# Kernel tuning notes

Hardware: AMD Instinct MI355X
Metric: run time of the kernel (lower is better)

The kernel has to match this reference:

```python
import jax, jax.numpy as jnp
import numpy as np

N_NODES = 100000
N_EDGES = 3200000
N_GRAPHS = 128
HIDDEN = 128
DEPTH = 3


def setup_inputs() -> dict:
    key = jax.random.key(0)
    ks = jax.random.split(key, 12)
    x = jax.random.normal(ks[0], (N_NODES, 1), dtype=jnp.float32)
    edge_index = jax.random.randint(ks[1], (2, N_EDGES), 0, N_NODES, dtype=jnp.int64)
    batch = jnp.sort(jax.random.randint(ks[2], (N_NODES,), 0, N_GRAPHS, dtype=jnp.int64))
    s = 1.0 / np.sqrt(HIDDEN)
    return {
        "x": x,
        "edge_index": edge_index,
        "batch": batch,
        "W_emb": jax.random.normal(ks[3], (1, HIDDEN), dtype=jnp.float32),
        "b_emb": jax.random.normal(ks[4], (HIDDEN,), dtype=jnp.float32) * 0.01,
        "W_gnn": jax.random.normal(ks[5], (DEPTH, HIDDEN, HIDDEN), dtype=jnp.float32) * s,
        "b_gnn": jax.random.normal(ks[6], (DEPTH, HIDDEN), dtype=jnp.float32) * 0.01,
        "W_c1": jax.random.normal(ks[7], (HIDDEN, HIDDEN // 2), dtype=jnp.float32) * s,
        "b_c1": jax.random.normal(ks[8], (HIDDEN // 2,), dtype=jnp.float32) * 0.01,
        "W_c2": jax.random.normal(ks[9], (HIDDEN // 2, 1), dtype=jnp.float32) * s,
        "b_c2": jax.random.normal(ks[10], (1,), dtype=jnp.float32) * 0.01,
    }


def reference(x, edge_index, batch, W_emb, b_emb, W_gnn, b_gnn, W_c1, b_c1, W_c2, b_c2):
    # --- GCN normalization (self-loops + symmetric deg^-1/2) ---
    loop = jnp.arange(N_NODES, dtype=edge_index.dtype)
    row = jnp.concatenate([edge_index[0], loop])  # source nodes
    col = jnp.concatenate([edge_index[1], loop])  # target nodes
    deg = jax.ops.segment_sum(jnp.ones_like(col, dtype=jnp.float32), col, num_segments=N_NODES)
    dinv = jnp.where(deg > 0, jax.lax.rsqrt(jnp.maximum(deg, 1.0)), 0.0)
    norm = dinv[row] * dinv[col]  # [E+N]

    # --- node embedding ---
    h = x @ W_emb + b_emb  # [N, H]

    # --- GCN layers: linear -> gather -> normalize -> scatter-add -> bias -> relu ---
    for l in range(DEPTH):
        h_lin = h @ W_gnn[l]                       # [N, H]
        msgs = h_lin[row] * norm[:, None]          # [E+N, H]
        agg = jax.ops.segment_sum(msgs, col, num_segments=N_NODES)
        h = jax.nn.relu(agg + b_gnn[l])

    # --- global mean pool per graph ---
    counts = jax.ops.segment_sum(jnp.ones((N_NODES,), jnp.float32), batch, num_segments=N_GRAPHS)
    sums = jax.ops.segment_sum(h, batch, num_segments=N_GRAPHS)
    g = sums / jnp.maximum(counts, 1.0)[:, None]   # [G, H]

    # --- classifier (dropout is identity in eval) ---
    z = jax.nn.relu(g @ W_c1 + b_c1)
    out = jax.nn.sigmoid(z @ W_c2 + b_c2)          # [G, 1]
    return out.squeeze(-1)                          # [G]
```

## Files before the change

### kernel.cpp

```cpp
#include <hip/hip_runtime.h>
#include <math.h>

#define HID 128
#define CAP 96
#define TILE 2048
#define WCAP 6144

typedef unsigned int uint;
typedef unsigned short ushort;
typedef float f32x2 __attribute__((ext_vector_type(2)));
typedef float f32x4 __attribute__((ext_vector_type(4)));
typedef short bf16x8 __attribute__((ext_vector_type(8)));

__device__ inline ushort f2bf(float f) {
    uint u = __float_as_uint(f);
    return (ushort)((u + 0x7fffu + ((u >> 16) & 1u)) >> 16);
}
__device__ inline uint packbf(float a, float b) {
    return (uint)f2bf(a) | ((uint)f2bf(b) << 16);
}

__device__ inline f32x2 fp8lo(uint q) { return __builtin_amdgcn_cvt_pk_f32_fp8(q, false); }
__device__ inline f32x2 fp8hi(uint q) { return __builtin_amdgcn_cvt_pk_f32_fp8(q, true); }
__device__ inline uint pack4fp8(float a, float b, float c, float d) {
    int t = __builtin_amdgcn_cvt_pk_fp8_f32(a, b, 0, false);
    return (uint)__builtin_amdgcn_cvt_pk_fp8_f32(c, d, t, true);
}
__device__ inline long long as_i64(uint2 u) {
    union { uint2 a; long long b; } c;
    c.a = u;
    return c.b;
}


__global__ void __launch_bounds__(256) k_part(const int* __restrict__ row,
                                              const int* __restrict__ col,
                                              int* __restrict__ bukCur,
                                              uint* __restrict__ recs, int E, int nTiles,
                                              const float* __restrict__ W_emb,
                                              const float* __restrict__ b_emb,
                                              const float* __restrict__ W_gnn,
                                              float* __restrict__ u, float* __restrict__ v,
                                              uint2* __restrict__ wfrag) {
    __shared__ int hist[800];
    __shared__ int hist2[800];
    __shared__ uint base[800];
    int t = threadIdx.x;
    if ((int)blockIdx.x >= nTiles) {
        int b = blockIdx.x - nTiles;
        if (b < 16) {
            int gid = b * 256 + t;
            int l = gid >> 11;
            int rem = gid & 2047;
            int kb = rem >> 9;
            int nt = (rem >> 6) & 7;
            int lane = rem & 63;
            int k0 = kb * 32 + (lane >> 4) * 8;
            int n = nt * 16 + (lane & 15);
            const float* Wp = W_gnn + (size_t)(l + 1) * HID * HID;
            uint2 o;
            o.x = pack4fp8(Wp[(k0 + 0) * HID + n], Wp[(k0 + 1) * HID + n],
                           Wp[(k0 + 2) * HID + n], Wp[(k0 + 3) * HID + n]);
            o.y = pack4fp8(Wp[(k0 + 4) * HID + n], Wp[(k0 + 5) * HID + n],
                           Wp[(k0 + 6) * HID + n], Wp[(k0 + 7) * HID + n]);
            wfrag[gid] = o;
        } else if (t < HID) {
            float su = 0.f, sv = 0.f;
            for (int k = 0; k < HID; ++k) {
                float w = W_gnn[k * HID + t];
                su = fmaf(W_emb[k], w, su);
                sv = fmaf(b_emb[k], w, sv);
            }
            u[t] = su;
            v[t] = sv;
        }
        return;
    }
    for (int i = t; i < 800; i += 256) { hist[i] = 0; hist2[i] = 0; }
    __syncthreads();
    int i0 = blockIdx.x * TILE;
    int i1 = min(E, i0 + TILE);
    for (int i = i0 + t; i < i1; i += 256) {
        atomicAdd(&hist[col[i] >> 7], 1);
    }
    __syncthreads();
    for (int i = t; i < 800; i += 256)
        if (hist[i] > 0) base[i] = (uint)atomicAdd(&bukCur[i], hist[i]);
    __syncthreads();
    for (int i = i0 + t; i < i1; i += 256) {
        int c = col[i];
        int w = c >> 7;
        uint p = (uint)atomicAdd(&hist2[w], 1);
        uint idx = base[w] + p;
        if (idx < WCAP)
            recs[(size_t)w * WCAP + idx] = (uint)row[i] | ((uint)(c & 127) << 17);
    }
}


__global__ void __launch_bounds__(256) k_fbin(const uint* __restrict__ recs,
                                              const int* __restrict__ bukCur,
                                              const float* __restrict__ x,
                                              int* __restrict__ cnt,
                                              int* __restrict__ ebin,
                                              float* __restrict__ dinv,
                                              float2* __restrict__ pk0, int N) {
    __shared__ int lcnt[128];
    int w = blockIdx.x;
    int t = threadIdx.x;
    if (t < 128) lcnt[t] = 0;
    __syncthreads();
    int n = min(bukCur[w], WCAP);
    const uint* rp = recs + (size_t)w * WCAP;
    int cbase = w << 7;
    for (int j = t; j < n; j += 256) {
        uint u = rp[j];
        int r = (int)(u & 0x1FFFFu);
        int cl = (int)((u >> 17) & 127u);
        int p = atomicAdd(&lcnt[cl], 1);
        if (p < CAP) ebin[(size_t)(cbase + cl) * CAP + p] = r << 5;
    }
    __syncthreads();
    if (t < 128) {
        int c = cbase + t;
        if (c < N) {
            cnt[c] = lcnt[t];
            float d = rsqrtf((float)lcnt[t] + 1.0f);
            dinv[c] = d;
            pk0[c] = make_float2(d, d * x[c]);
        }
    }
}


__global__ void __launch_bounds__(256) k_sagg(const int* __restrict__ cnt,
                                              const int* __restrict__ ebin,
                                              const float* __restrict__ x,
                                              const float* __restrict__ dinv,
                                              const float2* __restrict__ pk0,
                                              const float* __restrict__ u,
                                              const float* __restrict__ v,
                                              const float* __restrict__ b0,
                                              uint* __restrict__ g8, int N) {
    __shared__ float sS0[16], sS1[16], sDc[16];
    int t = threadIdx.x;
    int qw = t >> 4;
    int ll = t & 15;
    int c0 = blockIdx.x * 16;
    int c = c0 + qw;
    float A = 0.f, B = 0.f;
    float dc = 0.f;
    if (c < N) {
        dc = dinv[c];
        int n = min(cnt[c], CAP);
        const int* bp = ebin + (size_t)c * CAP;
        int k = ll;
        for (; k + 16 < n; k += 32) {
            int o0 = bp[k], o1 = bp[k + 16];
            float2 p0 = pk0[o0 >> 5], p1 = pk0[o1 >> 5];
            A += p0.x + p1.x;
            B += p0.y + p1.y;
        }
        if (k < n) {
            float2 p = pk0[bp[k] >> 5];
            A += p.x;
            B += p.y;
        }
    }
#pragma unroll
    for (int m = 1; m <= 8; m <<= 1) {
        A += __shfl_xor(A, m);
        B += __shfl_xor(B, m);
    }
    if (ll == 0 && c < N) {
        float d2 = dc * dc;
        sS0[qw] = fmaf(dc, A, d2);
        sS1[qw] = fmaf(dc, B, d2 * x[c]);
        sDc[qw] = dc;
    }
    __syncthreads();
    int nloc = min(16, N - c0);
    int total = nloc * 32;
    for (int gid = t; gid < total; gid += 256) {
        int lc = gid >> 5;
        int j = (gid & 31) * 4;
        float t1 = sS1[lc], t0 = sS0[lc], dcc = sDc[lc];
        float v0 = fmaxf(fmaf(t1, u[j + 0], fmaf(t0, v[j + 0], b0[j + 0])), 0.f);
        float v1 = fmaxf(fmaf(t1, u[j + 1], fmaf(t0, v[j + 1], b0[j + 1])), 0.f);
        float v2 = fmaxf(fmaf(t1, u[j + 2], fmaf(t0, v[j + 2], b0[j + 2])), 0.f);
        float v3 = fmaxf(fmaf(t1, u[j + 3], fmaf(t0, v[j + 3], b0[j + 3])), 0.f);
        g8[(size_t)(c0 + lc) * 32 + (gid & 31)] = pack4fp8(dcc * v0, dcc * v1, dcc * v2, dcc * v3);
    }
}


__global__ void __launch_bounds__(256) k_agg(const int* __restrict__ cnt,
                                             const int* __restrict__ ebin,
                                             const float* __restrict__ dinv,
                                             const uint* __restrict__ g8,
                                             uint* __restrict__ a, int N) {
    int wave = (blockIdx.x * 256 + threadIdx.x) >> 6;
    if (wave >= N) return;
    int lane = threadIdx.x & 63;
    int c = wave;
    int ql = lane & 15;
    int qg = lane >> 4;
    const uint* __restrict__ gq = g8 + ql * 2;

    f32x2 a0 = {0.f, 0.f}, a1 = {0.f, 0.f}, a2 = {0.f, 0.f}, a3 = {0.f, 0.f};

    int n = min(cnt[c], CAP);
    int total = n + 1;
    const int* __restrict__ bp = ebin + (size_t)c * CAP - 1;

    for (int base = 0; base < total; base += 64) {
        int cw = min(total - base, 64);
        int gi = base + lane;
        int ro = 0;
        if (lane < cw) ro = (gi == 0) ? (c << 5) : bp[gi];
        int j = 0;
        for (; j + 16 <= cw; j += 16) {
            int o0 = __shfl(ro, j + qg);
            int o1 = __shfl(ro, j + 4 + qg);
            int o2 = __shfl(ro, j + 8 + qg);
            int o3 = __shfl(ro, j + 12 + qg);
            uint2 q0 = *(const uint2*)(gq + o0);
            uint2 q1 = *(const uint2*)(gq + o1);
            uint2 q2 = *(const uint2*)(gq + o2);
            uint2 q3 = *(const uint2*)(gq + o3);
            a0 += fp8lo(q0.x); a1 += fp8hi(q0.x); a2 += fp8lo(q0.y); a3 += fp8hi(q0.y);
            a0 += fp8lo(q1.x); a1 += fp8hi(q1.x); a2 += fp8lo(q1.y); a3 += fp8hi(q1.y);
            a0 += fp8lo(q2.x); a1 += fp8hi(q2.x); a2 += fp8lo(q2.y); a3 += fp8hi(q2.y);
            a0 += fp8lo(q3.x); a1 += fp8hi(q3.x); a2 += fp8lo(q3.y); a3 += fp8hi(q3.y);
        }
        for (; j + 4 <= cw; j += 4) {
            int o0 = __shfl(ro, j + qg);
            uint2 q0 = *(const uint2*)(gq + o0);
            a0 += fp8lo(q0.x); a1 += fp8hi(q0.x); a2 += fp8lo(q0.y); a3 += fp8hi(q0.y);
        }
        if (j < cw) {
            int e = j + qg;
            int o0 = __shfl(ro, min(e, cw - 1));
            uint2 q0 = *(const uint2*)(gq + o0);
            if (e >= cw) { q0.x = 0u; q0.y = 0u; }
            a0 += fp8lo(q0.x); a1 += fp8hi(q0.x); a2 += fp8lo(q0.y); a3 += fp8hi(q0.y);
        }
    }

    float r0 = a0.x, r1 = a0.y, r2 = a1.x, r3 = a1.y;
    float r4 = a2.x, r5 = a2.y, r6 = a3.x, r7 = a3.y;
#pragma unroll
    for (int m = 16; m <= 32; m <<= 1) {
        r0 += __shfl_xor(r0, m); r1 += __shfl_xor(r1, m);
        r2 += __shfl_xor(r2, m); r3 += __shfl_xor(r3, m);
        r4 += __shfl_xor(r4, m); r5 += __shfl_xor(r5, m);
        r6 += __shfl_xor(r6, m); r7 += __shfl_xor(r7, m);
    }
    if (qg == 0) {
        float dc = dinv[c];
        uint2 o;
        o.x = pack4fp8(dc * r0, dc * r1, dc * r2, dc * r3);
        o.y = pack4fp8(dc * r4, dc * r5, dc * r6, dc * r7);
        ((uint2*)(a + (size_t)c * 32))[ql] = o;
    }
}


#define RCH 32
__global__ void __launch_bounds__(256, 2) k_gemm(const uint* __restrict__ A,
                                                 const uint2* __restrict__ wfrag,
                                                 const float* __restrict__ bias,
                                                 const float* __restrict__ rowscale,
                                                 uint* __restrict__ H8, int N) {
    __shared__ uint2 sAf[4][2][64];
    __shared__ float sEp[4][16][68];
    int t = threadIdx.x;
    int w = t >> 6;
    int lane = t & 63;
    int rowgrp = w >> 1;
    int colh = w & 1;

    uint2 Bf[4][4];
#pragma unroll
    for (int kb = 0; kb < 4; ++kb)
#pragma unroll
        for (int i = 0; i < 4; ++i)
            Bf[kb][i] = wfrag[(kb * 8 + colh * 4 + i) * 64 + lane];

    float4 bb = ((const float4*)bias)[colh * 16 + (lane & 15)];

    int nchunk = (N + RCH - 1) / RCH;
    for (int ch = blockIdx.x; ch < nchunk; ch += gridDim.x) {
        int r0 = ch * RCH;
        __syncthreads();
        {
            int i = t;
#pragma unroll
            for (int s = 0; s < 2; ++s, i += 256) {
                int kb = i >> 7;
                int rg = (i >> 6) & 1;
                int ln = i & 63;
                int gr = r0 + rg * 16 + (ln & 15);
                gr = min(gr, N - 1);
                sAf[kb][rg][ln] = ((const uint2*)(A + (size_t)gr * 32))[kb * 4 + (ln >> 4)];
            }
        }
        __syncthreads();

        f32x4 acc[4] = {{0.f, 0.f, 0.f, 0.f}, {0.f, 0.f, 0.f, 0.f},
                        {0.f, 0.f, 0.f, 0.f}, {0.f, 0.f, 0.f, 0.f}};
#pragma unroll
        for (int kb = 0; kb < 4; ++kb) {
            long long af = as_i64(sAf[kb][rowgrp][lane]);
#pragma unroll
            for (int i = 0; i < 4; ++i)
                acc[i] = __builtin_amdgcn_mfma_f32_16x16x32_fp8_fp8(af, as_i64(Bf[kb][i]),
                                                                    acc[i], 0, 0, 0);
        }

#pragma unroll
        for (int i = 0; i < 4; ++i) {
#pragma unroll
            for (int reg = 0; reg < 4; ++reg)
                sEp[w][(lane >> 4) * 4 + reg][i * 16 + (lane & 15)] = acc[i][reg];
        }
#pragma unroll
        for (int e = 0; e < 4; ++e) {
            int rr = (lane >> 4) + 4 * e;
            int cu = lane & 15;
            const float* sp = &sEp[w][rr][cu * 4];
            int rowg = r0 + rowgrp * 16 + rr;
            if (rowg < N) {
                float sc = rowscale ? rowscale[rowg] : 1.0f;
                float o0 = sc * fmaxf(sp[0] + bb.x, 0.f);
                float o1 = sc * fmaxf(sp[1] + bb.y, 0.f);
                float o2 = sc * fmaxf(sp[2] + bb.z, 0.f);
                float o3 = sc * fmaxf(sp[3] + bb.w, 0.f);
                H8[(size_t)rowg * 32 + colh * 16 + cu] = pack4fp8(o0, o1, o2, o3);
            }
        }
    }
}



__global__ void k_pool(const uint* __restrict__ h8, const int* __restrict__ batch,
                       float* __restrict__ gpp, float* __restrict__ gcnt, int N) {
    __shared__ float sp[128];
    int gi = blockIdx.x >> 2, part = blockIdx.x & 3;
    int G = gridDim.x >> 2;
    int t = threadIdx.x;
    int ui = t & 31;
    int sub = t >> 5;
    sp[t] = 0.f;
    __syncthreads();
    int lo = 0, hi = N;
    while (lo < hi) { int m = (lo + hi) >> 1; if (batch[m] < gi) lo = m + 1; else hi = m; }
    int start = lo;
    lo = start; hi = N;
    while (lo < hi) { int m = (lo + hi) >> 1; if (batch[m] <= gi) lo = m + 1; else hi = m; }
    int end = lo;
    if (part == 0 && t == 0) gcnt[gi] = (float)(end - start);
    int len = end - start;
    int q = (len + 15) >> 4;
    int seg = part * 4 + sub;
    int rs = start + seg * q;
    int re = min(end, rs + q);
    float s0 = 0.f, s1 = 0.f, s2 = 0.f, s3 = 0.f;
    for (int i = rs; i < re; ++i) {
        uint qq = h8[(size_t)i * 32 + ui];
        f32x2 lo2 = fp8lo(qq), hi2 = fp8hi(qq);
        s0 += lo2.x; s1 += lo2.y; s2 += hi2.x; s3 += hi2.y;
    }
    if (re > rs) {
        atomicAdd(&sp[ui * 4 + 0], s0);
        atomicAdd(&sp[ui * 4 + 1], s1);
        atomicAdd(&sp[ui * 4 + 2], s2);
        atomicAdd(&sp[ui * 4 + 3], s3);
    }
    __syncthreads();
    gpp[((size_t)part * G + gi) * 128 + t] = sp[t];
}

__global__ void k_cls(const float* __restrict__ gpp, const float* __restrict__ gcnt,
                      const float* __restrict__ Wc1, const float* __restrict__ bc1,
                      const float* __restrict__ Wc2, const float* __restrict__ bc2,
                      float* __restrict__ out, int G) {
    __shared__ float sg[128];
    int g = blockIdx.x;
    int j = threadIdx.x;
    float inv = 1.0f / fmaxf(gcnt[g], 1.0f);
    for (int k = j; k < 128; k += 64) {
        float s = gpp[((size_t)0 * G + g) * 128 + k] + gpp[((size_t)1 * G + g) * 128 + k] +
                  gpp[((size_t)2 * G + g) * 128 + k] + gpp[((size_t)3 * G + g) * 128 + k];
        sg[k] = s * inv;
    }
    __syncthreads();
    float z = bc1[j];
    for (int k = 0; k < HID; ++k) z = fmaf(sg[k], Wc1[k * 64 + j], z);
    z = fmaxf(z, 0.f);
    float p = z * Wc2[j];
    for (int off = 32; off; off >>= 1) p += __shfl_down(p, off);
    if (j == 0) out[g] = 1.0f / (1.0f + expf(-(p + bc2[0])));
}


extern "C" void kernel_launch(void* const* d_in, const int* in_sizes, int n_in,
                              void* d_out, int out_size, void* d_ws, size_t ws_size,
                              hipStream_t stream) {
    const float* x     = (const float*)d_in[0];
    const int*   eidx  = (const int*)d_in[1];
    const int*   batch = (const int*)d_in[2];
    const float* W_emb = (const float*)d_in[3];
    const float* b_emb = (const float*)d_in[4];
    const float* W_gnn = (const float*)d_in[5];
    const float* b_gnn = (const float*)d_in[6];
    const float* W_c1  = (const float*)d_in[7];
    const float* b_c1  = (const float*)d_in[8];
    const float* W_c2  = (const float*)d_in[9];
    const float* b_c2  = (const float*)d_in[10];

    const int N = in_sizes[0];
    const int E = in_sizes[1] / 2;
    const int G = out_size;
    const int* row = eidx;
    const int* col = eidx + E;
    const int NWIN = (N + 127) >> 7;

    char* ws = (char*)d_ws;
    auto alloc = [&](size_t bytes) -> void* {
        void* p = (void*)ws;
        ws += (bytes + 255) & ~(size_t)255;
        return p;
    };
    int*    cnt    = (int*)alloc((size_t)N * 4);
    float*  dinv   = (float*)alloc((size_t)N * 4);
    float2* pk0    = (float2*)alloc((size_t)N * 8);
    int*    bukCur = (int*)alloc((size_t)NWIN * 4);
    uint*   recs   = (uint*)alloc((size_t)NWIN * WCAP * 4);
    int*    ebin   = (int*)alloc((size_t)N * CAP * 4);
    float*  u      = (float*)alloc(HID * 4);
    float*  v      = (float*)alloc(HID * 4);
    uint*   G8     = (uint*)alloc((size_t)N * 32 * 4);
    uint*   A      = (uint*)alloc((size_t)N * 32 * 4);
    uint2*  wfrag  = (uint2*)alloc(4096 * 8);
    float*  gpp    = (float*)alloc((size_t)4 * G * HID * 4);
    float*  gcnt   = (float*)alloc((size_t)G * 4);

    hipMemsetAsync(bukCur, 0, (size_t)NWIN * 4, stream);

    int nTiles = (E + TILE - 1) / TILE;
    k_part<<<nTiles + 17, 256, 0, stream>>>(row, col, bukCur, recs, E, nTiles,
                                            W_emb, b_emb, W_gnn, u, v, wfrag);
    k_fbin<<<NWIN, 256, 0, stream>>>(recs, bukCur, x, cnt, ebin, dinv, pk0, N);

    k_sagg<<<(N + 15) / 16, 256, 0, stream>>>(cnt, ebin, x, dinv, pk0, u, v, b_gnn, G8, N);

    int nchunk = (N + RCH - 1) / RCH;
    int gblk = nchunk < 768 ? nchunk : 768;
    for (int l = 1; l < 3; ++l) {
        k_agg<<<(N + 3) / 4, 256, 0, stream>>>(cnt, ebin, dinv, G8, A, N);
        k_gemm<<<gblk, 256, 0, stream>>>(A, wfrag + (size_t)(l - 1) * 2048,
                                         b_gnn + (size_t)l * HID,
                                         (l == 1) ? dinv : (const float*)nullptr,
                                         G8, N);
    }

    k_pool<<<G * 4, 128, 0, stream>>>(G8, batch, gpp, gcnt, N);
    k_cls<<<G, 64, 0, stream>>>(gpp, gcnt, W_c1, b_c1, W_c2, b_c2, (float*)d_out, G);
}
```

Before: 388.4 us.

## Replace two-pass window partitioning with direct per-node global atomic binning

Removes the two-stage bucket partition (block-local histograms into 128-node windows, then per-window re-binning in shared memory) and instead has each edge atomically increment the global count of its target node and write straight into that node's bin. A small kernel then computes dinv and pk0 from the counts. This drops one kernel, the intermediate record buffer, and its extra read/write pass. In exchange it issues millions of global atomics on random addresses and scatters writes across the whole ebin array, which may cost more than the shared-memory atomics it replaces.

```diff
diff --git a/kernel.cpp b/kernel.cpp
--- a/kernel.cpp
+++ b/kernel.cpp
@@ -3,8 +3,6 @@
 
 #define HID 128
 #define CAP 96
-#define TILE 2048
-#define WCAP 6144
 
 typedef unsigned int uint;
 typedef unsigned short ushort;
@@ -33,21 +31,18 @@
 }
 
 
-__global__ void __launch_bounds__(256) k_part(const int* __restrict__ row,
-                                              const int* __restrict__ col,
-                                              int* __restrict__ bukCur,
-                                              uint* __restrict__ recs, int E, int nTiles,
-                                              const float* __restrict__ W_emb,
-                                              const float* __restrict__ b_emb,
-                                              const float* __restrict__ W_gnn,
-                                              float* __restrict__ u, float* __restrict__ v,
-                                              uint2* __restrict__ wfrag) {
-    __shared__ int hist[800];
-    __shared__ int hist2[800];
-    __shared__ uint base[800];
+__global__ void __launch_bounds__(256) k_bin(const int* __restrict__ row,
+                                             const int* __restrict__ col,
+                                             int* __restrict__ cnt,
+                                             int* __restrict__ ebin, int E, int nEB,
+                                             const float* __restrict__ W_emb,
+                                             const float* __restrict__ b_emb,
+                                             const float* __restrict__ W_gnn,
+                                             float* __restrict__ u, float* __restrict__ v,
+                                             uint2* __restrict__ wfrag) {
     int t = threadIdx.x;
-    if ((int)blockIdx.x >= nTiles) {
-        int b = blockIdx.x - nTiles;
+    if ((int)blockIdx.x >= nEB) {
+        int b = blockIdx.x - nEB;
         if (b < 16) {
             int gid = b * 256 + t;
             int l = gid >> 11;
@@ -76,59 +71,24 @@
         }
         return;
     }
-    for (int i = t; i < 800; i += 256) { hist[i] = 0; hist2[i] = 0; }
-    __syncthreads();
-    int i0 = blockIdx.x * TILE;
-    int i1 = min(E, i0 + TILE);
-    for (int i = i0 + t; i < i1; i += 256) {
-        atomicAdd(&hist[col[i] >> 7], 1);
-    }
-    __syncthreads();
-    for (int i = t; i < 800; i += 256)
-        if (hist[i] > 0) base[i] = (uint)atomicAdd(&bukCur[i], hist[i]);
-    __syncthreads();
-    for (int i = i0 + t; i < i1; i += 256) {
+    int stride = nEB * 256;
+    for (int i = blockIdx.x * 256 + t; i < E; i += stride) {
         int c = col[i];
-        int w = c >> 7;
-        uint p = (uint)atomicAdd(&hist2[w], 1);
-        uint idx = base[w] + p;
-        if (idx < WCAP)
-            recs[(size_t)w * WCAP + idx] = (uint)row[i] | ((uint)(c & 127) << 17);
-    }
-}
-
-
-__global__ void __launch_bounds__(256) k_fbin(const uint* __restrict__ recs,
-                                              const int* __restrict__ bukCur,
+        int r = row[i];
+        int p = atomicAdd(&cnt[c], 1);
+        if (p < CAP) ebin[(size_t)c * CAP + p] = r << 5;
+    }
+}
+
+__global__ void __launch_bounds__(256) k_prep(const int* __restrict__ cnt,
                                               const float* __restrict__ x,
-                                              int* __restrict__ cnt,
-                                              int* __restrict__ ebin,
                                               float* __restrict__ dinv,
                                               float2* __restrict__ pk0, int N) {
-    __shared__ int lcnt[128];
-    int w = blockIdx.x;
-    int t = threadIdx.x;
-    if (t < 128) lcnt[t] = 0;
-    __syncthreads();
-    int n = min(bukCur[w], WCAP);
-    const uint* rp = recs + (size_t)w * WCAP;
-    int cbase = w << 7;
-    for (int j = t; j < n; j += 256) {
-        uint u = rp[j];
-        int r = (int)(u & 0x1FFFFu);
-        int cl = (int)((u >> 17) & 127u);
-        int p = atomicAdd(&lcnt[cl], 1);
-        if (p < CAP) ebin[(size_t)(cbase + cl) * CAP + p] = r << 5;
-    }
-    __syncthreads();
-    if (t < 128) {
-        int c = cbase + t;
-        if (c < N) {
-            cnt[c] = lcnt[t];
-            float d = rsqrtf((float)lcnt[t] + 1.0f);
-            dinv[c] = d;
-            pk0[c] = make_float2(d, d * x[c]);
-        }
+    int c = blockIdx.x * 256 + threadIdx.x;
+    if (c < N) {
+        float d = rsqrtf((float)cnt[c] + 1.0f);
+        dinv[c] = d;
+        pk0[c] = make_float2(d, d * x[c]);
     }
 }
 
@@ -425,7 +385,6 @@
     const int G = out_size;
     const int* row = eidx;
     const int* col = eidx + E;
-    const int NWIN = (N + 127) >> 7;
 
     char* ws = (char*)d_ws;
     auto alloc = [&](size_t bytes) -> void* {
@@ -436,8 +395,6 @@
     int*    cnt    = (int*)alloc((size_t)N * 4);
     float*  dinv   = (float*)alloc((size_t)N * 4);
     float2* pk0    = (float2*)alloc((size_t)N * 8);
-    int*    bukCur = (int*)alloc((size_t)NWIN * 4);
-    uint*   recs   = (uint*)alloc((size_t)NWIN * WCAP * 4);
     int*    ebin   = (int*)alloc((size_t)N * CAP * 4);
     float*  u      = (float*)alloc(HID * 4);
     float*  v      = (float*)alloc(HID * 4);
@@ -447,12 +404,12 @@
     float*  gpp    = (float*)alloc((size_t)4 * G * HID * 4);
     float*  gcnt   = (float*)alloc((size_t)G * 4);
 
-    hipMemsetAsync(bukCur, 0, (size_t)NWIN * 4, stream);
-
-    int nTiles = (E + TILE - 1) / TILE;
-    k_part<<<nTiles + 17, 256, 0, stream>>>(row, col, bukCur, recs, E, nTiles,
-                                            W_emb, b_emb, W_gnn, u, v, wfrag);
-    k_fbin<<<NWIN, 256, 0, stream>>>(recs, bukCur, x, cnt, ebin, dinv, pk0, N);
+    hipMemsetAsync(cnt, 0, (size_t)N * 4, stream);
+
+    int nEB = 2048;
+    k_bin<<<nEB + 17, 256, 0, stream>>>(row, col, cnt, ebin, E, nEB,
+                                        W_emb, b_emb, W_gnn, u, v, wfrag);
+    k_prep<<<(N + 255) / 256, 256, 0, stream>>>(cnt, x, dinv, pk0, N);
 
     k_sagg<<<(N + 15) / 16, 256, 0, stream>>>(cnt, ebin, x, dinv, pk0, u, v, b_gnn, G8, N);
 
```

Measured after the change: 545.5 us. 1.4x slower.
